# Optimization experiments

Hardware: AMD Instinct MI355X
Metric: run time of the kernel (lower is better)

## Reference

```python
import jax, jax.numpy as jnp
import numpy as np

N = 4096
D_IN = 512
D_OUT = 512

def setup_inputs() -> dict:
    key = jax.random.key(0)
    k1, k2, k3 = jax.random.split(key, 3)
    X = jax.random.normal(k1, (N, D_IN), dtype=jnp.float32)
    A = jax.random.uniform(k2, (N, N), dtype=jnp.float32)
    # Linear(input_dim, output_dim, bias=False): W is [out, in], y = x @ W.T
    W = jax.random.normal(k3, (D_OUT, D_IN), dtype=jnp.float32) * (1.0 / np.sqrt(D_IN))
    return {"X": X, "A": A, "W": W}

def reference(X, A, W):
    # A2 = A + I
    A2 = A + jnp.eye(A.shape[0], dtype=A.dtype)
    # Dhat = diag(diagonal(A2)); fractional_matrix_power(Dhat, -1/2) on a
    # diagonal matrix is elementwise d^{-1/2}; dense diag GEMMs reduce to
    # row/column scaling.
    dscale = jnp.diagonal(A2) ** (-0.5)  # [N]
    temp = (A2 @ X) @ W.T                # [N, D_OUT]
    A_norm = dscale[:, None] * A2 * dscale[None, :]  # D^-1/2 A2 D^-1/2
    return jax.nn.relu(A_norm @ temp)
```

## Files before the change

kernel.cpp:

```cpp
#include <hip/hip_runtime.h>
#include <hip/hip_bf16.h>
#include <stdint.h>

typedef float  f32x4  __attribute__((ext_vector_type(4)));
typedef __bf16 bf16x8 __attribute__((ext_vector_type(8)));
typedef unsigned short us4 __attribute__((ext_vector_type(4)));

#define NDIM 4096
#define DDIM 512
#define PSTRIDE 2097152
#define NPART 4

__device__ __forceinline__ unsigned short f2bf(float f) {
    union { float f; uint32_t u; } v; v.f = f;
    uint32_t u = v.u;
    u += 0x7FFFu + ((u >> 16) & 1u);
    return (unsigned short)(u >> 16);
}

__device__ __forceinline__ float b2f(unsigned short s) {
    union { uint32_t u; float f; } v; v.u = (uint32_t)s << 16; return v.f;
}

__device__ __forceinline__ f32x4 us4tof(us4 u) {
    f32x4 r; r.x = b2f(u.x); r.y = b2f(u.y); r.z = b2f(u.z); r.w = b2f(u.w);
    return r;
}

__global__ void prep_kernel(const float* __restrict__ A, const float* __restrict__ X,
                            const float* __restrict__ W,
                            unsigned short* __restrict__ A2, unsigned short* __restrict__ Xb,
                            unsigned short* __restrict__ Wb, float* __restrict__ ds) {
    const int b = blockIdx.x, tid = threadIdx.x;
    if (b < 16384) {
        int i = b * 256 + tid;
        int e = i << 2;
        int row = e >> 12, col = e & 4095;
        f32x4 v = ((const f32x4*)A)[i];
        int d = row - col;
        if (d >= 0 && d < 4) v[d] += 1.0f;
        us4 o; o.x = f2bf(v.x); o.y = f2bf(v.y); o.z = f2bf(v.z); o.w = f2bf(v.w);
        ((us4*)A2)[i] = o;
    } else if (b < 18432) {
        int i = (b - 16384) * 256 + tid;
        f32x4 v = ((const f32x4*)X)[i];
        us4 o; o.x = f2bf(v.x); o.y = f2bf(v.y); o.z = f2bf(v.z); o.w = f2bf(v.w);
        ((us4*)Xb)[i] = o;
    } else if (b < 18688) {
        int i = (b - 18432) * 256 + tid;
        f32x4 v = ((const f32x4*)W)[i];
        us4 o; o.x = f2bf(v.x); o.y = f2bf(v.y); o.z = f2bf(v.z); o.w = f2bf(v.w);
        ((us4*)Wb)[i] = o;
    } else {
        int i = (b - 18688) * 256 + tid;
        if (i < NDIM) ds[i] = rsqrtf(A[(size_t)i * (NDIM + 1)] + 1.0f);
    }
}

template <int MODE, int SWAP>
__global__ __launch_bounds__(256, 2) void gemm_bt(
    const unsigned short* __restrict__ A,
    const unsigned short* __restrict__ B,
    void* __restrict__ C,
    int K, int kc, int ldc)
{
    __shared__ unsigned short lsA[128 * 128];
    __shared__ unsigned short lsB[128 * 128];

    const int tid  = threadIdx.x;
    const int wid  = tid >> 6;
    const int lane = tid & 63;
    const int m0 = (SWAP ? blockIdx.y : blockIdx.x) * 128;
    const int n0 = (SWAP ? blockIdx.x : blockIdx.y) * 128;
    const int kbase = blockIdx.z * kc;
    const int wm = (wid & 1) * 64;
    const int wn = (wid >> 1) * 64;
    const int quad = lane >> 4;
    const int c16  = lane & 15;

    const int lr    = lane >> 4;
    const int chunk = lane & 15;
    const int offe = ((chunk ^ lr) * 16);

    f32x4 acc[4][4];
    #pragma unroll
    for (int i = 0; i < 4; i++)
        #pragma unroll
        for (int j = 0; j < 4; j++) acc[i][j] = (f32x4)0.0f;

    const char* gA = (const char*)A + ((size_t)(m0 + wid * 32 + lr) * K) * 2;
    const char* gB = (const char*)B + ((size_t)(n0 + wid * 32 + lr) * K) * 2;
    const size_t rowstep = (size_t)4 * K * 2;

    for (int k0 = kbase; k0 < kbase + kc; k0 += 128) {
        const size_t kb = (size_t)k0 * 2;
        #pragma unroll
        for (int i = 0; i < 8; i++) {
            const size_t src = kb + (size_t)i * rowstep + (size_t)(offe ^ ((i & 1) << 6));
            __builtin_amdgcn_global_load_lds(
                (const __attribute__((address_space(1))) void*)(gA + src),
                (__attribute__((address_space(3))) void*)(&lsA[(wid * 8 + i) * 512]),
                16, 0, 0);
            __builtin_amdgcn_global_load_lds(
                (const __attribute__((address_space(1))) void*)(gB + src),
                (__attribute__((address_space(3))) void*)(&lsB[(wid * 8 + i) * 512]),
                16, 0, 0);
        }
        __syncthreads();

        #pragma unroll
        for (int ks = 0; ks < 4; ks++) {
            bf16x8 bfrag[4], afrag[4];
            #pragma unroll
            for (int nt = 0; nt < 4; nt++) {
                int r = wn + nt * 16 + c16;
                int pc = (quad + ks * 4) ^ (r & 7);
                bfrag[nt] = *(const bf16x8*)((const char*)lsB + r * 256 + pc * 16);
            }
            #pragma unroll
            for (int mt = 0; mt < 4; mt++) {
                int r = wm + mt * 16 + c16;
                int pc = (quad + ks * 4) ^ (r & 7);
                afrag[mt] = *(const bf16x8*)((const char*)lsA + r * 256 + pc * 16);
            }
            #pragma unroll
            for (int mt = 0; mt < 4; mt++)
                #pragma unroll
                for (int nt = 0; nt < 4; nt++)
                    acc[mt][nt] = __builtin_amdgcn_mfma_f32_16x16x32_bf16(
                        afrag[mt], bfrag[nt], acc[mt][nt], 0, 0, 0);
        }
        __syncthreads();
    }

    #pragma unroll
    for (int mt = 0; mt < 4; mt++) {
        const int gm0 = m0 + wm + mt * 16 + quad * 4;
        #pragma unroll
        for (int nt = 0; nt < 4; nt++) {
            const int gn = n0 + wn + nt * 16 + c16;
            f32x4 v = acc[mt][nt];
            if (MODE == 0) {
                us4 o;
                o.x = f2bf(v.x); o.y = f2bf(v.y); o.z = f2bf(v.z); o.w = f2bf(v.w);
                *(us4*)((unsigned short*)C + (size_t)gn * ldc + gm0) = o;
            } else {
                unsigned short* o = (unsigned short*)C + (size_t)blockIdx.z * PSTRIDE
                                  + (size_t)gm0 * ldc + gn;
                o[0]               = f2bf(v.x);
                o[ldc]             = f2bf(v.y);
                o[2 * (size_t)ldc] = f2bf(v.z);
                o[3 * (size_t)ldc] = f2bf(v.w);
            }
        }
    }
}

__global__ void ep2_kernel(const unsigned short* __restrict__ P, const float* __restrict__ ds,
                           unsigned short* __restrict__ T2) {
    int t = blockIdx.x * 256 + threadIdx.x;
    int e = t << 2;
    int i = e & 4095;
    f32x4 v = us4tof(((const us4*)P)[t]);
    #pragma unroll
    for (int z = 1; z < NPART; z++)
        v += us4tof(((const us4*)(P + (size_t)z * PSTRIDE))[t]);
    f32x4 d = *(const f32x4*)(ds + i);
    us4 o;
    o.x = f2bf(v.x * d.x); o.y = f2bf(v.y * d.y);
    o.z = f2bf(v.z * d.z); o.w = f2bf(v.w * d.w);
    ((us4*)T2)[t] = o;
}

__global__ void ep3_kernel(const unsigned short* __restrict__ Q, const float* __restrict__ ds,
                           float* __restrict__ out) {
    int t = blockIdx.x * 256 + threadIdx.x;
    int e = t << 2;
    int i = e >> 9;
    float s = ds[i];
    f32x4 v = us4tof(((const us4*)Q)[t]);
    #pragma unroll
    for (int z = 1; z < NPART; z++)
        v += us4tof(((const us4*)(Q + (size_t)z * PSTRIDE))[t]);
    f32x4 o;
    o.x = fmaxf(v.x * s, 0.0f); o.y = fmaxf(v.y * s, 0.0f);
    o.z = fmaxf(v.z * s, 0.0f); o.w = fmaxf(v.w * s, 0.0f);
    ((f32x4*)out)[t] = o;
}

extern "C" void kernel_launch(void* const* d_in, const int* in_sizes, int n_in,
                              void* d_out, int out_size, void* d_ws, size_t ws_size,
                              hipStream_t stream) {
    const float* X = (const float*)d_in[0];
    const float* A = (const float*)d_in[1];
    const float* W = (const float*)d_in[2];

    char* ws = (char*)d_ws;
    float*          dsc  = (float*)ws;
    unsigned short* A2   = (unsigned short*)(ws + 16384);
    unsigned short* Xb   = (unsigned short*)(ws + 33570816u);
    unsigned short* Wb   = (unsigned short*)(ws + 37765120u);
    unsigned short* Yt   = (unsigned short*)(ws + 38289408u);
    unsigned short* T2   = (unsigned short*)(ws + 42483712u);
    unsigned short* Part = (unsigned short*)(ws + 46678016u);

    prep_kernel<<<18704, 256, 0, stream>>>(A, X, W, A2, Xb, Wb, dsc);

    gemm_bt<0, 0><<<dim3(32, 4, 1), 256, 0, stream>>>(Xb, Wb, Yt, 512, 512, 4096);
    gemm_bt<2, 1><<<dim3(32, 4, NPART), 256, 0, stream>>>(Yt, A2, Part, 4096, 4096 / NPART, 4096);
    ep2_kernel<<<2048, 256, 0, stream>>>(Part, dsc, T2);
    gemm_bt<2, 0><<<dim3(32, 4, NPART), 256, 0, stream>>>(A2, T2, Part, 4096, 4096 / NPART, 512);
    ep3_kernel<<<2048, 256, 0, stream>>>(Part, dsc, (float*)d_out);
}
```

Measured before the change: 167.3 us.

## Add double-buffered 256x256 GEMM kernel with phased prefetch for big GEMMs

```diff
diff --git a/kernel.cpp b/kernel.cpp
--- a/kernel.cpp
+++ b/kernel.cpp
@@ -9,7 +9,7 @@
 #define NDIM 4096
 #define DDIM 512
 #define PSTRIDE 2097152
-#define NPART 4
+#define NPART 8
 
 __device__ __forceinline__ unsigned short f2bf(float f) {
     union { float f; uint32_t u; } v; v.f = f;
@@ -156,6 +156,136 @@
     }
 }
 
+#define VMW(n)  asm volatile("s_waitcnt vmcnt(" #n ")" ::: "memory")
+#define LGKM0   asm volatile("s_waitcnt lgkmcnt(0)" ::: "memory")
+#define SBAR    __builtin_amdgcn_s_barrier()
+#define SCH0    __builtin_amdgcn_sched_barrier(0)
+#define GLB(src, dst) __builtin_amdgcn_global_load_lds( \
+    (const __attribute__((address_space(1))) void*)(src), \
+    (__attribute__((address_space(3))) void*)(dst), 16, 0, 0)
+#define DSR(off) (*(const bf16x8*)(ldsc + (off)))
+
+#define PHASE(p, vm, STMT) do {                                               \
+    VMW(vm); SBAR; SCH0;                                                      \
+    bf16x8 a00 = DSR(bo + baseA0 + (2*(p))*2048);                             \
+    bf16x8 a01 = DSR(bo + baseA1 + (2*(p))*2048);                             \
+    bf16x8 a10 = DSR(bo + baseA0 + (2*(p)+1)*2048);                           \
+    bf16x8 a11 = DSR(bo + baseA1 + (2*(p)+1)*2048);                           \
+    if ((p) == 0) {                                                           \
+        _Pragma("unroll")                                                     \
+        for (int nt = 0; nt < 4; nt++) {                                      \
+            fb0[nt] = DSR(bo + baseB0 + nt*2048);                             \
+            fb1[nt] = DSR(bo + baseB1 + nt*2048);                             \
+        }                                                                     \
+    }                                                                         \
+    STMT                                                                      \
+    LGKM0; SCH0;                                                              \
+    __builtin_amdgcn_s_setprio(1);                                            \
+    _Pragma("unroll")                                                         \
+    for (int nt = 0; nt < 4; nt++) {                                          \
+        acc[2*(p)][nt]   = __builtin_amdgcn_mfma_f32_16x16x32_bf16(a00, fb0[nt], acc[2*(p)][nt], 0, 0, 0);   \
+        acc[2*(p)][nt]   = __builtin_amdgcn_mfma_f32_16x16x32_bf16(a01, fb1[nt], acc[2*(p)][nt], 0, 0, 0);   \
+        acc[2*(p)+1][nt] = __builtin_amdgcn_mfma_f32_16x16x32_bf16(a10, fb0[nt], acc[2*(p)+1][nt], 0, 0, 0); \
+        acc[2*(p)+1][nt] = __builtin_amdgcn_mfma_f32_16x16x32_bf16(a11, fb1[nt], acc[2*(p)+1][nt], 0, 0, 0); \
+    }                                                                         \
+    __builtin_amdgcn_s_setprio(0);                                            \
+} while (0)
+
+template <int SWAP>
+__global__ __launch_bounds__(512, 2) void gemm256_bt(
+    const unsigned short* __restrict__ A,
+    const unsigned short* __restrict__ B,
+    unsigned short* __restrict__ C,
+    int K, int kc, int ldc)
+{
+    __shared__ unsigned short lds[65536];
+
+    const int tid  = threadIdx.x;
+    const int wid  = tid >> 6;
+    const int lane = tid & 63;
+    const int m0 = (SWAP ? blockIdx.y : blockIdx.x) * 256;
+    const int n0 = (SWAP ? blockIdx.x : blockIdx.y) * 256;
+    const int kbase = blockIdx.z * kc;
+
+    const int wm = (wid >> 2) * 128;
+    const int wn = (wid & 3) * 64;
+    const int quad = lane >> 4;
+    const int c16  = lane & 15;
+    const int keyq = c16 & 7;
+
+    const char* ldsc = (const char*)lds;
+
+    const int baseA0 = (wm + c16) * 128 + ((quad ^ keyq) * 16);
+    const int baseA1 = baseA0 ^ 64;
+    const int baseB0 = 32768 + (wn + c16) * 128 + ((quad ^ keyq) * 16);
+    const int baseB1 = baseB0 ^ 64;
+
+    const int lr3 = lane >> 3, ch8 = lane & 7;
+    const int srcx = ((ch8 ^ lr3) << 4);
+    const char* gA = (const char*)A
+        + ((size_t)(m0 + (wid & 3) * 8 + (wid >> 2) * 128 + lr3) * K + kbase) * 2 + srcx;
+    const char* gB = (const char*)B
+        + ((size_t)(n0 + wid * 8 + lr3) * K + kbase) * 2 + srcx;
+    const size_t stepA = (size_t)32 * K * 2;
+    const size_t stepB = (size_t)64 * K * 2;
+
+    const int dAo = (wid & 3) * 512 + (wid >> 2) * 8192;
+    const int dBo = 16384 + wid * 512;
+
+    f32x4 acc[8][4];
+    #pragma unroll
+    for (int i = 0; i < 8; i++)
+        #pragma unroll
+        for (int j = 0; j < 4; j++) acc[i][j] = (f32x4)0.0f;
+
+    const int T = kc >> 6;
+
+    #pragma unroll
+    for (int j = 0; j < 4; j++) GLB(gB + (size_t)j * stepB, &lds[dBo + j * 4096]);
+    #pragma unroll
+    for (int i = 0; i < 4; i++) GLB(gA + (size_t)i * stepA, &lds[dAo + i * 2048]);
+
+    int bo = 0;
+    for (int kt = 0; kt < T - 1; ++kt) {
+        const char* sA = gA + (size_t)(kt + 1) * 128;
+        const char* sB = gB + (size_t)(kt + 1) * 128;
+        const int sb = (bo ^ 65536) >> 1;
+        bf16x8 fb0[4], fb1[4];
+        PHASE(0, 3, { GLB(sB,                     &lds[sb + dBo]);
+                      GLB(sB + stepB,             &lds[sb + dBo + 4096]); });
+        PHASE(1, 4, { GLB(sB + 2 * stepB,         &lds[sb + dBo + 8192]);
+                      GLB(sB + 3 * stepB,         &lds[sb + dBo + 12288]); });
+        PHASE(2, 5, { GLB(sA,                     &lds[sb + dAo]);
+                      GLB(sA + stepA,             &lds[sb + dAo + 2048]); });
+        PHASE(3, 6, { GLB(sA + 2 * stepA,         &lds[sb + dAo + 4096]);
+                      GLB(sA + 3 * stepA,         &lds[sb + dAo + 6144]); });
+        bo ^= 65536;
+    }
+    {
+        bf16x8 fb0[4], fb1[4];
+        PHASE(0, 3, );
+        PHASE(1, 2, );
+        PHASE(2, 1, );
+        PHASE(3, 0, );
+    }
+
+    unsigned short* Cp = C + (size_t)blockIdx.z * PSTRIDE;
+    #pragma unroll
+    for (int mt = 0; mt < 8; mt++) {
+        const int gm0 = m0 + wm + mt * 16 + quad * 4;
+        #pragma unroll
+        for (int nt = 0; nt < 4; nt++) {
+            const int gn = n0 + wn + nt * 16 + c16;
+            f32x4 v = acc[mt][nt];
+            unsigned short* o = Cp + (size_t)gm0 * ldc + gn;
+            o[0]               = f2bf(v.x);
+            o[ldc]             = f2bf(v.y);
+            o[2 * (size_t)ldc] = f2bf(v.z);
+            o[3 * (size_t)ldc] = f2bf(v.w);
+        }
+    }
+}
+
 __global__ void ep2_kernel(const unsigned short* __restrict__ P, const float* __restrict__ ds,
                            unsigned short* __restrict__ T2) {
     int t = blockIdx.x * 256 + threadIdx.x;
@@ -207,8 +337,8 @@
     prep_kernel<<<18704, 256, 0, stream>>>(A, X, W, A2, Xb, Wb, dsc);
 
     gemm_bt<0, 0><<<dim3(32, 4, 1), 256, 0, stream>>>(Xb, Wb, Yt, 512, 512, 4096);
-    gemm_bt<2, 1><<<dim3(32, 4, NPART), 256, 0, stream>>>(Yt, A2, Part, 4096, 4096 / NPART, 4096);
+    gemm256_bt<1><<<dim3(16, 2, NPART), 512, 0, stream>>>(Yt, A2, Part, 4096, 4096 / NPART, 4096);
     ep2_kernel<<<2048, 256, 0, stream>>>(Part, dsc, T2);
-    gemm_bt<2, 0><<<dim3(32, 4, NPART), 256, 0, stream>>>(A2, T2, Part, 4096, 4096 / NPART, 512);
+    gemm256_bt<0><<<dim3(16, 2, NPART), 512, 0, stream>>>(A2, T2, Part, 4096, 4096 / NPART, 512);
     ep3_kernel<<<2048, 256, 0, stream>>>(Part, dsc, (float*)d_out);
 }
```

Result: slower. 176.5 us (+5.5%).

## Add double-buffered full-width GEMM kernel for the two big N×N products

Applied to the files above, without the earlier changes.

```diff
diff --git a/kernel.cpp b/kernel.cpp
--- a/kernel.cpp
+++ b/kernel.cpp
@@ -9,7 +9,7 @@
 #define NDIM 4096
 #define DDIM 512
 #define PSTRIDE 2097152
-#define NPART 4
+#define NPART 8
 
 __device__ __forceinline__ unsigned short f2bf(float f) {
     union { float f; uint32_t u; } v; v.f = f;
@@ -156,6 +156,110 @@
     }
 }
 
+template <int BM, int BN, int WM, int WN>
+__global__ __launch_bounds__(512, 2) void gemm_thin(
+    const unsigned short* __restrict__ A,
+    const unsigned short* __restrict__ B,
+    unsigned short* __restrict__ C,
+    int K, int kc, int ldc)
+{
+    constexpr int ABYTES = BM * 64;
+    constexpr int BBYTES = BN * 64;
+    constexpr int BUFB   = ABYTES + BBYTES;
+    constexpr int TM = BM / WM / 16;
+    constexpr int TN = BN / WN / 16;
+    constexpr int IA = BM / 128;
+    constexpr int IB = BN / 128;
+
+    __shared__ char lds[2 * BUFB];
+
+    const int tid  = threadIdx.x;
+    const int wid  = tid >> 6;
+    const int lane = tid & 63;
+    const int m0 = (BM == 512) ? 0 : blockIdx.x * BM;
+    const int n0 = (BN == 512) ? 0 : blockIdx.x * BN;
+    const int kbase = blockIdx.z * kc;
+
+    const int wr = wid / WN, wc = wid % WN;
+    const int wm = wr * (TM * 16);
+    const int wn = wc * (TN * 16);
+    const int quad = lane >> 4;
+    const int c16  = lane & 15;
+
+    const int srow = lane >> 2, schunk = lane & 3;
+    const char* gAl = (const char*)A
+        + ((size_t)(m0 + wid * (BM / 8) + srow) * K + kbase) * 2 + schunk * 16;
+    const char* gBl = (const char*)B
+        + ((size_t)(n0 + wid * (BN / 8) + srow) * K + kbase) * 2 + schunk * 16;
+    const size_t rst16 = (size_t)16 * K * 2;
+
+    const int dA = wid * (BM / 8) * 64;
+    const int dB = ABYTES + wid * (BN / 8) * 64;
+
+    f32x4 acc[TM][TN];
+    #pragma unroll
+    for (int i = 0; i < TM; i++)
+        #pragma unroll
+        for (int j = 0; j < TN; j++) acc[i][j] = (f32x4)0.0f;
+
+    const int T = kc >> 5;
+
+#define GLB(src, dst) __builtin_amdgcn_global_load_lds( \
+    (const __attribute__((address_space(1))) void*)(src), \
+    (__attribute__((address_space(3))) void*)(dst), 16, 0, 0)
+
+    #pragma unroll
+    for (int i = 0; i < IA; i++) GLB(gAl + (size_t)i * rst16, lds + dA + i * 1024);
+    #pragma unroll
+    for (int i = 0; i < IB; i++) GLB(gBl + (size_t)i * rst16, lds + dB + i * 1024);
+    __syncthreads();
+
+    int bo = 0;
+    for (int t = 0; t < T; ++t) {
+        if (t + 1 < T) {
+            const char* sa = gAl + (size_t)(t + 1) * 64;
+            const char* sb = gBl + (size_t)(t + 1) * 64;
+            const int ob = bo ^ BUFB;
+            #pragma unroll
+            for (int i = 0; i < IA; i++) GLB(sa + (size_t)i * rst16, lds + ob + dA + i * 1024);
+            #pragma unroll
+            for (int i = 0; i < IB; i++) GLB(sb + (size_t)i * rst16, lds + ob + dB + i * 1024);
+        }
+        bf16x8 af[TM], bfr[TN];
+        #pragma unroll
+        for (int mt = 0; mt < TM; mt++)
+            af[mt] = *(const bf16x8*)(lds + bo + (wm + mt * 16 + c16) * 64 + quad * 16);
+        #pragma unroll
+        for (int nt = 0; nt < TN; nt++)
+            bfr[nt] = *(const bf16x8*)(lds + bo + ABYTES + (wn + nt * 16 + c16) * 64 + quad * 16);
+        #pragma unroll
+        for (int mt = 0; mt < TM; mt++)
+            #pragma unroll
+            for (int nt = 0; nt < TN; nt++)
+                acc[mt][nt] = __builtin_amdgcn_mfma_f32_16x16x32_bf16(
+                    af[mt], bfr[nt], acc[mt][nt], 0, 0, 0);
+        __syncthreads();
+        bo ^= BUFB;
+    }
+#undef GLB
+
+    unsigned short* Cp = C + (size_t)blockIdx.z * PSTRIDE;
+    #pragma unroll
+    for (int mt = 0; mt < TM; mt++) {
+        const int gm0 = m0 + wm + mt * 16 + quad * 4;
+        #pragma unroll
+        for (int nt = 0; nt < TN; nt++) {
+            const int gn = n0 + wn + nt * 16 + c16;
+            f32x4 v = acc[mt][nt];
+            unsigned short* o = Cp + (size_t)gm0 * ldc + gn;
+            o[0]               = f2bf(v.x);
+            o[ldc]             = f2bf(v.y);
+            o[2 * (size_t)ldc] = f2bf(v.z);
+            o[3 * (size_t)ldc] = f2bf(v.w);
+        }
+    }
+}
+
 __global__ void ep2_kernel(const unsigned short* __restrict__ P, const float* __restrict__ ds,
                            unsigned short* __restrict__ T2) {
     int t = blockIdx.x * 256 + threadIdx.x;
@@ -207,8 +311,10 @@
     prep_kernel<<<18704, 256, 0, stream>>>(A, X, W, A2, Xb, Wb, dsc);
 
     gemm_bt<0, 0><<<dim3(32, 4, 1), 256, 0, stream>>>(Xb, Wb, Yt, 512, 512, 4096);
-    gemm_bt<2, 1><<<dim3(32, 4, NPART), 256, 0, stream>>>(Yt, A2, Part, 4096, 4096 / NPART, 4096);
+    gemm_thin<512, 128, 4, 2><<<dim3(32, 1, NPART), 512, 0, stream>>>(
+        Yt, A2, Part, 4096, 4096 / NPART, 4096);
     ep2_kernel<<<2048, 256, 0, stream>>>(Part, dsc, T2);
-    gemm_bt<2, 0><<<dim3(32, 4, NPART), 256, 0, stream>>>(A2, T2, Part, 4096, 4096 / NPART, 512);
+    gemm_thin<128, 512, 2, 4><<<dim3(32, 1, NPART), 512, 0, stream>>>(
+        A2, T2, Part, 4096, 4096 / NPART, 512);
     ep3_kernel<<<2048, 256, 0, stream>>>(Part, dsc, (float*)d_out);
 }
```

New measurement: 185.3 us. 1.11x slower.
